# Performance work log

Hardware: AMD Instinct MI355X
Metric: run time of the kernel (lower is better)

The kernel has to match this reference:

```python
import jax, jax.numpy as jnp
import numpy as np

MD_S = 1
MD_R = 16
EVAL_STEPS = 7
INV_T = 100.0
EPS = 1e-6

B, C, S = 16, 512, 4096  # batch, channels, flattened spatial


def setup_inputs() -> dict:
    key = jax.random.key(0)
    k1, k2 = jax.random.split(key)
    x = jax.random.uniform(k1, (B, C, S), dtype=jnp.float32)  # non-negative input for NMF
    bases = jax.random.uniform(k2, (B * MD_S, S, MD_R), dtype=jnp.float32)
    # F.normalize(bases, dim=1)
    bases = bases / (jnp.linalg.norm(bases, axis=1, keepdims=True) + 1e-12)
    return {"x": x, "bases": bases}


def _nmf_step(xm, bases, coef):
    # xm: (BS, D, N), bases: (BS, D, R), coef: (BS, N, R)
    # multiplicative update for coef
    num = jnp.einsum('bdn,bdr->bnr', xm, bases)
    den = jnp.einsum('bnr,brs->bns', coef, jnp.einsum('bdr,bds->brs', bases, bases))
    coef = coef * num / (den + EPS)
    # multiplicative update for bases
    num = jnp.einsum('bdn,bnr->bdr', xm, coef)
    den = jnp.einsum('bdr,brs->bds', bases, jnp.einsum('bnr,bns->brs', coef, coef))
    bases = bases * num / (den + EPS)
    return bases, coef


def _local_inference(xm, bases):
    # coef init: softmax(inv_t * x^T bases)
    coef = jax.nn.softmax(INV_T * jnp.einsum('bdn,bdr->bnr', xm, bases), axis=-1)

    def body(carry, _):
        b, c = _nmf_step(xm, carry[0], carry[1])
        return (b, c), None

    (bases, coef), _ = jax.lax.scan(body, (bases, coef), None, length=EVAL_STEPS)
    return bases, coef


def reference(x, bases):
    Bb, Cc, Ss = x.shape
    D = Ss
    N = Cc // MD_S
    xm = x.reshape(Bb * MD_S, N, D).transpose(0, 2, 1)  # (BS, D, N)

    bases_i, coef_i = jax.lax.stop_gradient(_local_inference(xm, bases))

    # compute_coef (differentiable in the original module)
    num = jnp.einsum('bdn,bdr->bnr', xm, bases_i)
    den = jnp.einsum('bnr,brs->bns', coef_i, jnp.einsum('bdr,bds->brs', bases_i, bases_i))
    coef = coef_i * num / (den + EPS)

    # x_rec = bases @ coef^T -> (BS, D, N) -> transpose -> (B, C, S)
    out = jnp.einsum('bdr,bnr->bdn', bases_i, coef)
    out = out.transpose(0, 2, 1).reshape(Bb, Cc, Ss)
    return out
```

## Files before the change

### kernel.cpp

```cpp
#include <hip/hip_runtime.h>

#define EPS 1e-6f

template <int CTRL>
__device__ __forceinline__ float dpp_add(float v) {
  int moved = __builtin_amdgcn_update_dpp(0, __float_as_int(v), CTRL, 0xF, 0xF, false);
  return v + __int_as_float(moved);
}

__global__ __launch_bounds__(256, 4) void kernelA(
    const float* __restrict__ x, const float* __restrict__ bases,
    float* __restrict__ Ppart, float* __restrict__ CtC)
{
  __shared__ __align__(16) float lb[512 * 16];
  const int tid = threadIdx.x;
  const int grp = blockIdx.x;
  const int b = blockIdx.y;
  const int h = blockIdx.z;
  if (h == 0 && grp == 0) CtC[b * 256 + tid] = 0.0f;
  const int w = tid >> 6;
  const int lane = tid & 63;
  const int rot = lane & 3;
  const int n0 = grp * 16 + w * 4;
  const float* __restrict__ xp = x + ((size_t)(b * 512 + n0)) * 4096 + h * 2048;
  const float4* __restrict__ srcf4 =
      (const float4*)(bases + ((size_t)(b * 4096 + h * 2048)) * 16);

  float acc[4][16];
#pragma unroll
  for (int i = 0; i < 4; ++i)
#pragma unroll
    for (int r = 0; r < 16; ++r) acc[i][r] = 0.0f;

  for (int c = 0; c < 4; ++c) {
#pragma unroll
    for (int k = 0; k < 8; ++k) {
      int idx = k * 256 + tid;
      int dl = idx >> 2, q = idx & 3;
      int pos = ((q + (dl >> 2)) & 3) * 4;
      *(float4*)(&lb[dl * 16 + pos]) = srcf4[(c * 512 + dl) * 4 + q];
    }
    __syncthreads();
    const float* __restrict__ xpc = xp + c * 512;
#pragma unroll
    for (int j = 0; j < 2; ++j) {
      const int d0 = j * 256 + lane * 4;
      float xr[4][4];
#pragma unroll
      for (int i = 0; i < 4; ++i) {
        float4 t = *(const float4*)(xpc + (size_t)i * 4096 + d0);
        xr[i][0] = t.x; xr[i][1] = t.y; xr[i][2] = t.z; xr[i][3] = t.w;
      }
#pragma unroll
      for (int k = 0; k < 4; ++k) {
        const float* __restrict__ br = &lb[(d0 + k) * 16];
        float4 bq0 = *(const float4*)(br + (((0 + rot) & 3) * 4));
        float4 bq1 = *(const float4*)(br + (((1 + rot) & 3) * 4));
        float4 bq2 = *(const float4*)(br + (((2 + rot) & 3) * 4));
        float4 bq3 = *(const float4*)(br + (((3 + rot) & 3) * 4));
#pragma unroll
        for (int i = 0; i < 4; ++i) {
          const float xf = xr[i][k];
          acc[i][0]  = fmaf(xf, bq0.x, acc[i][0]);
          acc[i][1]  = fmaf(xf, bq0.y, acc[i][1]);
          acc[i][2]  = fmaf(xf, bq0.z, acc[i][2]);
          acc[i][3]  = fmaf(xf, bq0.w, acc[i][3]);
          acc[i][4]  = fmaf(xf, bq1.x, acc[i][4]);
          acc[i][5]  = fmaf(xf, bq1.y, acc[i][5]);
          acc[i][6]  = fmaf(xf, bq1.z, acc[i][6]);
          acc[i][7]  = fmaf(xf, bq1.w, acc[i][7]);
          acc[i][8]  = fmaf(xf, bq2.x, acc[i][8]);
          acc[i][9]  = fmaf(xf, bq2.y, acc[i][9]);
          acc[i][10] = fmaf(xf, bq2.z, acc[i][10]);
          acc[i][11] = fmaf(xf, bq2.w, acc[i][11]);
          acc[i][12] = fmaf(xf, bq3.x, acc[i][12]);
          acc[i][13] = fmaf(xf, bq3.y, acc[i][13]);
          acc[i][14] = fmaf(xf, bq3.z, acc[i][14]);
          acc[i][15] = fmaf(xf, bq3.w, acc[i][15]);
        }
      }
    }
    __syncthreads();
  }

#pragma unroll
  for (int i = 0; i < 4; ++i)
#pragma unroll
    for (int r = 0; r < 16; ++r) {
      float v = acc[i][r];
      v = dpp_add<0x121>(v);
      v = dpp_add<0x122>(v);
      v = dpp_add<0x124>(v);
      v = dpp_add<0x128>(v);
      v += __shfl_xor(v, 16, 64);
      v += __shfl_xor(v, 32, 64);
      acc[i][r] = v;
    }

  if (lane == 0) {
    float* __restrict__ pp =
        Ppart + (((size_t)(h * 16 + b)) * 512 + n0) * 16;
#pragma unroll
    for (int i = 0; i < 4; ++i) {
#pragma unroll
      for (int q = 0; q < 4; ++q)
        *(float4*)(pp + i * 16 + q * 4) =
            make_float4(acc[i][q * 4], acc[i][q * 4 + 1], acc[i][q * 4 + 2], acc[i][q * 4 + 3]);
    }
  }
}

__global__ __launch_bounds__(256) void kernelSM(
    const float* __restrict__ Ppart, float* __restrict__ coef)
{
  const int gid = blockIdx.x * 256 + threadIdx.x;
  const int b = gid >> 9, n = gid & 511;
  const float* __restrict__ p0 = Ppart + (((size_t)b) * 512 + n) * 16;
  const float* __restrict__ p1 = Ppart + (((size_t)(16 + b)) * 512 + n) * 16;
  float p[16];
#pragma unroll
  for (int r = 0; r < 16; ++r) p[r] = p0[r] + p1[r];
  float m = p[0];
#pragma unroll
  for (int r = 1; r < 16; ++r) m = fmaxf(m, p[r]);
  float e[16];
  float s = 0.0f;
#pragma unroll
  for (int r = 0; r < 16; ++r) { e[r] = __expf(100.0f * (p[r] - m)); s += e[r]; }
  float inv = 1.0f / s;
  float* __restrict__ crow = coef + (((size_t)b) * 512 + n) * 16;
#pragma unroll
  for (int r = 0; r < 16; ++r) crow[r] = e[r] * inv;
}

__global__ __launch_bounds__(256) void kernelGram(
    const float* __restrict__ M, float* __restrict__ out, int L)
{
  __shared__ __align__(16) float sm[256 * 20];
  __shared__ __align__(16) float part[4 * 272];
  const int tid = threadIdx.x;
  const int b = blockIdx.y;
  const int sl = blockIdx.x;
  const float4* __restrict__ src = (const float4*)(M + ((size_t)b * L + (size_t)sl * 256) * 16);
#pragma unroll
  for (int k = 0; k < 4; ++k) {
    int idx = k * 256 + tid;
    int row = idx >> 2, q = idx & 3;
    *(float4*)(&sm[row * 20 + q * 4]) = src[idx];
  }
  __syncthreads();
  const int rq = tid & 3;
  const int s = (tid >> 2) & 15;
  const int g = tid >> 6;
  float a0 = 0.f, a1 = 0.f, a2 = 0.f, a3 = 0.f;
#pragma unroll 4
  for (int l = g * 64; l < g * 64 + 64; ++l) {
    float4 bv = *(const float4*)(&sm[l * 20 + rq * 4]);
    float cs = sm[l * 20 + s];
    a0 = fmaf(cs, bv.x, a0);
    a1 = fmaf(cs, bv.y, a1);
    a2 = fmaf(cs, bv.z, a2);
    a3 = fmaf(cs, bv.w, a3);
  }
  *(float4*)(&part[g * 272 + s * 16 + rq * 4]) = make_float4(a0, a1, a2, a3);
  __syncthreads();
  float v = part[0 * 272 + tid] + part[1 * 272 + tid] + part[2 * 272 + tid] + part[3 * 272 + tid];
  atomicAdd(out + b * 256 + tid, v);
}

__global__ __launch_bounds__(256) void kernelCU(
    float* __restrict__ coef, const float* __restrict__ Ppart,
    const float* __restrict__ BtBr, float* __restrict__ BtBz,
    float* __restrict__ CtCadd)
{
  __shared__ __align__(16) float sm[256 * 20 + 4 * 272];
  const int tid = threadIdx.x;
  BtBz[blockIdx.x * 128 + (tid & 127)] = 0.0f;
  const int b = blockIdx.x >> 1;
  const int n = ((blockIdx.x & 1) << 8) + tid;
  float* __restrict__ crow = coef + ((size_t)(b * 512 + n)) * 16;
  const float* __restrict__ p0 = Ppart + (((size_t)b) * 512 + n) * 16;
  const float* __restrict__ p1 = Ppart + (((size_t)(16 + b)) * 512 + n) * 16;
  const float* __restrict__ btb = BtBr + b * 256;
  float cv[16], den[16];
#pragma unroll
  for (int r = 0; r < 16; ++r) cv[r] = crow[r];
#pragma unroll
  for (int r = 0; r < 16; ++r) den[r] = 0.f;
#pragma unroll
  for (int s2 = 0; s2 < 16; ++s2) {
    const float bs = cv[s2];
#pragma unroll
    for (int r = 0; r < 16; ++r) den[r] = fmaf(bs, btb[s2 * 16 + r], den[r]);
  }
#pragma unroll
  for (int r = 0; r < 16; ++r) {
    float cn = cv[r] * (p0[r] + p1[r]) / (den[r] + EPS);
    crow[r] = cn;
    sm[tid * 20 + r] = cn;
  }
  __syncthreads();
  const int rq = tid & 3;
  const int s = (tid >> 2) & 15;
  const int g = tid >> 6;
  float a0 = 0.f, a1 = 0.f, a2 = 0.f, a3 = 0.f;
#pragma unroll 4
  for (int l = g * 64; l < g * 64 + 64; ++l) {
    float4 bv = *(const float4*)(&sm[l * 20 + rq * 4]);
    float cs = sm[l * 20 + s];
    a0 = fmaf(cs, bv.x, a0);
    a1 = fmaf(cs, bv.y, a1);
    a2 = fmaf(cs, bv.z, a2);
    a3 = fmaf(cs, bv.w, a3);
  }
  float* part = sm + 5120;
  *(float4*)(&part[g * 272 + s * 16 + rq * 4]) = make_float4(a0, a1, a2, a3);
  __syncthreads();
  float v = part[0 * 272 + tid] + part[1 * 272 + tid] + part[2 * 272 + tid] + part[3 * 272 + tid];
  atomicAdd(CtCadd + b * 256 + tid, v);
}

__global__ __launch_bounds__(256) void kernelBacc(
    const float* __restrict__ x, const float* __restrict__ coef,
    float* __restrict__ qpart)
{
  const int tid = threadIdx.x;
  const int dt = blockIdx.x, ns = blockIdx.y, b = blockIdx.z;
  const int d = dt * 512 + tid * 2;
  const float* __restrict__ xp = x + ((size_t)(b * 512 + ns * 128)) * 4096 + d;
  const float* __restrict__ cp = coef + ((size_t)(b * 512 + ns * 128)) * 16;
  float acc[2][16];
#pragma unroll
  for (int r = 0; r < 16; ++r) { acc[0][r] = 0.f; acc[1][r] = 0.f; }
#pragma unroll 4
  for (int n = 0; n < 128; ++n) {
    const float2 xv = *(const float2*)(xp + (size_t)n * 4096);
    const float* __restrict__ crow = cp + n * 16;
#pragma unroll
    for (int r = 0; r < 16; ++r) {
      acc[0][r] = fmaf(xv.x, crow[r], acc[0][r]);
      acc[1][r] = fmaf(xv.y, crow[r], acc[1][r]);
    }
  }
  float* __restrict__ qp = qpart + (((size_t)(ns * 16 + b)) * 4096 + d) * 16;
#pragma unroll
  for (int q = 0; q < 4; ++q)
    *(float4*)(qp + q * 4) = make_float4(acc[0][q * 4], acc[0][q * 4 + 1], acc[0][q * 4 + 2], acc[0][q * 4 + 3]);
#pragma unroll
  for (int q = 0; q < 4; ++q)
    *(float4*)(qp + 16 + q * 4) = make_float4(acc[1][q * 4], acc[1][q * 4 + 1], acc[1][q * 4 + 2], acc[1][q * 4 + 3]);
}

__global__ __launch_bounds__(256) void kernelBfin(
    const float* __restrict__ qpart, float* __restrict__ bases,
    const float* __restrict__ CtC, float* __restrict__ BtBadd)
{
  __shared__ __align__(16) float sm[256 * 20 + 4 * 272];
  const int tid = threadIdx.x;
  const int dt = blockIdx.x, b = blockIdx.y;
  const int d = dt * 256 + tid;
  float acc[16];
#pragma unroll
  for (int r = 0; r < 16; ++r) acc[r] = 0.f;
#pragma unroll
  for (int ns = 0; ns < 4; ++ns) {
    const float* __restrict__ qp = qpart + (((size_t)(ns * 16 + b)) * 4096 + d) * 16;
#pragma unroll
    for (int q = 0; q < 4; ++q) {
      float4 v = *(const float4*)(qp + q * 4);
      acc[q * 4 + 0] += v.x; acc[q * 4 + 1] += v.y; acc[q * 4 + 2] += v.z; acc[q * 4 + 3] += v.w;
    }
  }
  float* __restrict__ brow = bases + ((size_t)(b * 4096 + d)) * 16;
  float bv[16];
#pragma unroll
  for (int r = 0; r < 16; ++r) bv[r] = brow[r];
  const float* __restrict__ ctc = CtC + b * 256;
  float den[16];
#pragma unroll
  for (int r = 0; r < 16; ++r) den[r] = 0.f;
#pragma unroll
  for (int s2 = 0; s2 < 16; ++s2) {
    const float bs = bv[s2];
#pragma unroll
    for (int r = 0; r < 16; ++r) den[r] = fmaf(bs, ctc[s2 * 16 + r], den[r]);
  }
#pragma unroll
  for (int r = 0; r < 16; ++r) {
    float bn = bv[r] * acc[r] / (den[r] + EPS);
    brow[r] = bn;
    sm[tid * 20 + r] = bn;
  }
  __syncthreads();
  const int rq = tid & 3;
  const int s = (tid >> 2) & 15;
  const int g = tid >> 6;
  float a0 = 0.f, a1 = 0.f, a2 = 0.f, a3 = 0.f;
#pragma unroll 4
  for (int l = g * 64; l < g * 64 + 64; ++l) {
    float4 bq = *(const float4*)(&sm[l * 20 + rq * 4]);
    float cs = sm[l * 20 + s];
    a0 = fmaf(cs, bq.x, a0);
    a1 = fmaf(cs, bq.y, a1);
    a2 = fmaf(cs, bq.z, a2);
    a3 = fmaf(cs, bq.w, a3);
  }
  float* part = sm + 5120;
  *(float4*)(&part[g * 272 + s * 16 + rq * 4]) = make_float4(a0, a1, a2, a3);
  __syncthreads();
  float v = part[0 * 272 + tid] + part[1 * 272 + tid] + part[2 * 272 + tid] + part[3 * 272 + tid];
  atomicAdd(BtBadd + b * 256 + tid, v);
}

__global__ __launch_bounds__(256) void kernelOut(
    const float* __restrict__ bases, const float* __restrict__ coef,
    float* __restrict__ out)
{
  const int tid = threadIdx.x;
  const int dt = blockIdx.x, ns = blockIdx.y, b = blockIdx.z;
  const int d0 = dt * 1024 + tid * 4;
  float bv[4][16];
#pragma unroll
  for (int k = 0; k < 4; ++k) {
    const float* __restrict__ brow = bases + ((size_t)(b * 4096 + d0 + k)) * 16;
#pragma unroll
    for (int r = 0; r < 16; ++r) bv[k][r] = brow[r];
  }
  const float* __restrict__ cp = coef + ((size_t)(b * 512 + ns * 32)) * 16;
  float* __restrict__ op = out + ((size_t)(b * 512 + ns * 32)) * 4096 + d0;
#pragma unroll 4
  for (int n = 0; n < 32; ++n) {
    const float* __restrict__ crow = cp + n * 16;
    float v[4];
#pragma unroll
    for (int k = 0; k < 4; ++k) {
      float s = 0.f;
#pragma unroll
      for (int r = 0; r < 16; ++r) s = fmaf(bv[k][r], crow[r], s);
      v[k] = s;
    }
    *(float4*)(op + (size_t)n * 4096) = make_float4(v[0], v[1], v[2], v[3]);
  }
}

extern "C" void kernel_launch(void* const* d_in, const int* in_sizes, int n_in,
                              void* d_out, int out_size, void* d_ws, size_t ws_size,
                              hipStream_t stream) {
  const float* x = (const float*)d_in[0];
  const float* bases_in = (const float*)d_in[1];
  float* out = (float*)d_out;
  float* ws = (float*)d_ws;

  float* bases = ws;
  float* coef  = bases + 1048576;
  float* Ppart = coef + 131072;
  float* btb0  = Ppart + 262144;
  float* btb1  = btb0 + 4096;
  float* ctc   = btb1 + 4096;
  float* qpart = ctc + 4096;
  float* btb[2] = {btb0, btb1};

  hipMemsetAsync(btb0, 0, 4096 * sizeof(float), stream);
  hipMemcpyAsync(bases, bases_in, 1048576 * sizeof(float),
                 hipMemcpyDeviceToDevice, stream);

  kernelA<<<dim3(32, 16, 2), 256, 0, stream>>>(x, bases, Ppart, ctc);
  kernelSM<<<32, 256, 0, stream>>>(Ppart, coef);
  kernelGram<<<dim3(16, 16), 256, 0, stream>>>(bases, btb0, 4096);

  for (int t = 0; t < 7; ++t) {
    if (t > 0) kernelA<<<dim3(32, 16, 2), 256, 0, stream>>>(x, bases, Ppart, ctc);
    kernelCU<<<32, 256, 0, stream>>>(coef, Ppart, btb[t & 1], btb[(t + 1) & 1], ctc);
    kernelBacc<<<dim3(8, 4, 16), 256, 0, stream>>>(x, coef, qpart);
    kernelBfin<<<dim3(16, 16), 256, 0, stream>>>(qpart, bases, ctc, btb[(t + 1) & 1]);
  }

  kernelA<<<dim3(32, 16, 2), 256, 0, stream>>>(x, bases, Ppart, ctc);
  kernelCU<<<32, 256, 0, stream>>>(coef, Ppart, btb[1], btb[0], ctc);
  kernelOut<<<dim3(4, 16, 16), 256, 0, stream>>>(bases, coef, out);
}
```

Baseline: 1.043 ms.

## Read bases directly from global in kernelA and halve per-thread work in kernelBacc

kernelA no longer stages bases chunks through shared memory with __syncthreads. Each lane now loads its bases rows straight from global memory and software-prefetches the next x float4s into registers. kernelBacc moves from two d columns per thread to one, doubling the grid to raise occupancy and parallelism. The risks are redundant global or L2 traffic for bases across the four waves of a block, and less x reuse per thread in kernelBacc.

```diff
diff --git a/kernel.cpp b/kernel.cpp
--- a/kernel.cpp
+++ b/kernel.cpp
@@ -12,7 +12,6 @@
     const float* __restrict__ x, const float* __restrict__ bases,
     float* __restrict__ Ppart, float* __restrict__ CtC)
 {
-  __shared__ __align__(16) float lb[512 * 16];
   const int tid = threadIdx.x;
   const int grp = blockIdx.x;
   const int b = blockIdx.y;
@@ -20,11 +19,11 @@
   if (h == 0 && grp == 0) CtC[b * 256 + tid] = 0.0f;
   const int w = tid >> 6;
   const int lane = tid & 63;
-  const int rot = lane & 3;
   const int n0 = grp * 16 + w * 4;
-  const float* __restrict__ xp = x + ((size_t)(b * 512 + n0)) * 4096 + h * 2048;
-  const float4* __restrict__ srcf4 =
-      (const float4*)(bases + ((size_t)(b * 4096 + h * 2048)) * 16);
+  const float* __restrict__ xp =
+      x + ((size_t)(b * 512 + n0)) * 4096 + h * 2048 + lane * 4;
+  const float4* __restrict__ bp =
+      (const float4*)(bases + ((size_t)(b * 4096 + h * 2048 + lane * 4)) * 16);
 
   float acc[4][16];
 #pragma unroll
@@ -32,55 +31,46 @@
 #pragma unroll
     for (int r = 0; r < 16; ++r) acc[i][r] = 0.0f;
 
-  for (int c = 0; c < 4; ++c) {
-#pragma unroll
-    for (int k = 0; k < 8; ++k) {
-      int idx = k * 256 + tid;
-      int dl = idx >> 2, q = idx & 3;
-      int pos = ((q + (dl >> 2)) & 3) * 4;
-      *(float4*)(&lb[dl * 16 + pos]) = srcf4[(c * 512 + dl) * 4 + q];
-    }
-    __syncthreads();
-    const float* __restrict__ xpc = xp + c * 512;
-#pragma unroll
-    for (int j = 0; j < 2; ++j) {
-      const int d0 = j * 256 + lane * 4;
-      float xr[4][4];
+  float4 xv[4], xn[4];
+#pragma unroll
+  for (int i = 0; i < 4; ++i) xv[i] = *(const float4*)(xp + (size_t)i * 4096);
+
+  for (int j = 0; j < 8; ++j) {
+    if (j < 7) {
+#pragma unroll
+      for (int i = 0; i < 4; ++i)
+        xn[i] = *(const float4*)(xp + (size_t)i * 4096 + (size_t)(j + 1) * 256);
+    }
+#pragma unroll
+    for (int k = 0; k < 4; ++k) {
+      const float4* __restrict__ brow = bp + (size_t)(j * 256 + k) * 4;
+      float4 bq0 = brow[0];
+      float4 bq1 = brow[1];
+      float4 bq2 = brow[2];
+      float4 bq3 = brow[3];
 #pragma unroll
       for (int i = 0; i < 4; ++i) {
-        float4 t = *(const float4*)(xpc + (size_t)i * 4096 + d0);
-        xr[i][0] = t.x; xr[i][1] = t.y; xr[i][2] = t.z; xr[i][3] = t.w;
+        const float xf = (&xv[i].x)[k];
+        acc[i][0]  = fmaf(xf, bq0.x, acc[i][0]);
+        acc[i][1]  = fmaf(xf, bq0.y, acc[i][1]);
+        acc[i][2]  = fmaf(xf, bq0.z, acc[i][2]);
+        acc[i][3]  = fmaf(xf, bq0.w, acc[i][3]);
+        acc[i][4]  = fmaf(xf, bq1.x, acc[i][4]);
+        acc[i][5]  = fmaf(xf, bq1.y, acc[i][5]);
+        acc[i][6]  = fmaf(xf, bq1.z, acc[i][6]);
+        acc[i][7]  = fmaf(xf, bq1.w, acc[i][7]);
+        acc[i][8]  = fmaf(xf, bq2.x, acc[i][8]);
+        acc[i][9]  = fmaf(xf, bq2.y, acc[i][9]);
+        acc[i][10] = fmaf(xf, bq2.z, acc[i][10]);
+        acc[i][11] = fmaf(xf, bq2.w, acc[i][11]);
+        acc[i][12] = fmaf(xf, bq3.x, acc[i][12]);
+        acc[i][13] = fmaf(xf, bq3.y, acc[i][13]);
+        acc[i][14] = fmaf(xf, bq3.z, acc[i][14]);
+        acc[i][15] = fmaf(xf, bq3.w, acc[i][15]);
       }
-#pragma unroll
-      for (int k = 0; k < 4; ++k) {
-        const float* __restrict__ br = &lb[(d0 + k) * 16];
-        float4 bq0 = *(const float4*)(br + (((0 + rot) & 3) * 4));
-        float4 bq1 = *(const float4*)(br + (((1 + rot) & 3) * 4));
-        float4 bq2 = *(const float4*)(br + (((2 + rot) & 3) * 4));
-        float4 bq3 = *(const float4*)(br + (((3 + rot) & 3) * 4));
-#pragma unroll
-        for (int i = 0; i < 4; ++i) {
-          const float xf = xr[i][k];
-          acc[i][0]  = fmaf(xf, bq0.x, acc[i][0]);
-          acc[i][1]  = fmaf(xf, bq0.y, acc[i][1]);
-          acc[i][2]  = fmaf(xf, bq0.z, acc[i][2]);
-          acc[i][3]  = fmaf(xf, bq0.w, acc[i][3]);
-          acc[i][4]  = fmaf(xf, bq1.x, acc[i][4]);
-          acc[i][5]  = fmaf(xf, bq1.y, acc[i][5]);
-          acc[i][6]  = fmaf(xf, bq1.z, acc[i][6]);
-          acc[i][7]  = fmaf(xf, bq1.w, acc[i][7]);
-          acc[i][8]  = fmaf(xf, bq2.x, acc[i][8]);
-          acc[i][9]  = fmaf(xf, bq2.y, acc[i][9]);
-          acc[i][10] = fmaf(xf, bq2.z, acc[i][10]);
-          acc[i][11] = fmaf(xf, bq2.w, acc[i][11]);
-          acc[i][12] = fmaf(xf, bq3.x, acc[i][12]);
-          acc[i][13] = fmaf(xf, bq3.y, acc[i][13]);
-          acc[i][14] = fmaf(xf, bq3.z, acc[i][14]);
-          acc[i][15] = fmaf(xf, bq3.w, acc[i][15]);
-        }
-      }
-    }
-    __syncthreads();
+    }
+#pragma unroll
+    for (int i = 0; i < 4; ++i) xv[i] = xn[i];
   }
 
 #pragma unroll
@@ -226,29 +216,23 @@
 {
   const int tid = threadIdx.x;
   const int dt = blockIdx.x, ns = blockIdx.y, b = blockIdx.z;
-  const int d = dt * 512 + tid * 2;
+  const int d = dt * 256 + tid;
   const float* __restrict__ xp = x + ((size_t)(b * 512 + ns * 128)) * 4096 + d;
   const float* __restrict__ cp = coef + ((size_t)(b * 512 + ns * 128)) * 16;
-  float acc[2][16];
-#pragma unroll
-  for (int r = 0; r < 16; ++r) { acc[0][r] = 0.f; acc[1][r] = 0.f; }
+  float acc[16];
+#pragma unroll
+  for (int r = 0; r < 16; ++r) acc[r] = 0.f;
 #pragma unroll 4
   for (int n = 0; n < 128; ++n) {
-    const float2 xv = *(const float2*)(xp + (size_t)n * 4096);
+    const float xv = xp[(size_t)n * 4096];
     const float* __restrict__ crow = cp + n * 16;
 #pragma unroll
-    for (int r = 0; r < 16; ++r) {
-      acc[0][r] = fmaf(xv.x, crow[r], acc[0][r]);
-      acc[1][r] = fmaf(xv.y, crow[r], acc[1][r]);
-    }
+    for (int r = 0; r < 16; ++r) acc[r] = fmaf(xv, crow[r], acc[r]);
   }
   float* __restrict__ qp = qpart + (((size_t)(ns * 16 + b)) * 4096 + d) * 16;
 #pragma unroll
   for (int q = 0; q < 4; ++q)
-    *(float4*)(qp + q * 4) = make_float4(acc[0][q * 4], acc[0][q * 4 + 1], acc[0][q * 4 + 2], acc[0][q * 4 + 3]);
-#pragma unroll
-  for (int q = 0; q < 4; ++q)
-    *(float4*)(qp + 16 + q * 4) = make_float4(acc[1][q * 4], acc[1][q * 4 + 1], acc[1][q * 4 + 2], acc[1][q * 4 + 3]);
+    *(float4*)(qp + q * 4) = make_float4(acc[q * 4], acc[q * 4 + 1], acc[q * 4 + 2], acc[q * 4 + 3]);
 }
 
 __global__ __launch_bounds__(256) void kernelBfin(
@@ -371,7 +355,7 @@
   for (int t = 0; t < 7; ++t) {
     if (t > 0) kernelA<<<dim3(32, 16, 2), 256, 0, stream>>>(x, bases, Ppart, ctc);
     kernelCU<<<32, 256, 0, stream>>>(coef, Ppart, btb[t & 1], btb[(t + 1) & 1], ctc);
-    kernelBacc<<<dim3(8, 4, 16), 256, 0, stream>>>(x, coef, qpart);
+    kernelBacc<<<dim3(16, 4, 16), 256, 0, stream>>>(x, coef, qpart);
     kernelBfin<<<dim3(16, 16), 256, 0, stream>>>(qpart, bases, ctc, btb[(t + 1) & 1]);
   }
 
```

After: 1.598 ms. +53.3%, slower.
